# Kernel tuning notes

Hardware: AMD Instinct MI355X
Metric: run time of the kernel (lower is better)

## Reference

```python
import jax, jax.numpy as jnp
import numpy as np

NUM_HEADS = 16
EMBED_DIM = 1024
SEQ_LEN = 2048
BATCH = 2


def setup_inputs() -> dict:
    key = jax.random.key(0)
    ks = jax.random.split(key, 7)
    E = EMBED_DIM
    scale = 1.0 / np.sqrt(E)
    return {
        "query": jax.random.normal(ks[0], (SEQ_LEN, BATCH, E), jnp.float32),
        "key": jax.random.normal(ks[1], (SEQ_LEN, BATCH, E), jnp.float32),
        "value": jax.random.normal(ks[2], (SEQ_LEN, BATCH, E), jnp.float32),
        "in_proj_weight": jax.random.normal(ks[3], (3 * E, E), jnp.float32) * scale,
        "in_proj_bias": jnp.zeros((3 * E,), jnp.float32),
        "out_proj_weight": jax.random.normal(ks[4], (E, E), jnp.float32) * scale,
        "out_proj_bias": jnp.zeros((E,), jnp.float32),
    }


def reference(query, key, value, in_proj_weight, in_proj_bias, out_proj_weight, out_proj_bias):
    T, B, E = query.shape
    H = NUM_HEADS
    d = E // H
    scaling = float(d) ** -0.5
    # in-projections: rows [0:E) -> q, [E:2E) -> k, [2E:3E) -> v
    q = query @ in_proj_weight[:E].T + in_proj_bias[:E]
    k = key @ in_proj_weight[E:2 * E].T + in_proj_bias[E:2 * E]
    v = value @ in_proj_weight[2 * E:].T + in_proj_bias[2 * E:]
    q = q * scaling
    # (T, B, E) -> (B*H, T, d)
    q = q.reshape(T, B * H, d).transpose(1, 0, 2)
    k = k.reshape(T, B * H, d).transpose(1, 0, 2)
    v = v.reshape(T, B * H, d).transpose(1, 0, 2)
    S = k.shape[1]
    scores = jnp.einsum('ntd,nsd->nts', q, k)  # (B*H, T, S)
    attn = jax.nn.softmax(scores, axis=-1)
    out = jnp.einsum('nts,nsd->ntd', attn, v)  # (B*H, T, d)
    out = out.transpose(1, 0, 2).reshape(T, B, E)
    out = out @ out_proj_weight.T + out_proj_bias
    attn_avg = attn.reshape(B, H, T, S).sum(axis=1) / H
    return out, attn_avg
```

## Files before the change

kernel.cpp:

```cpp
#include <hip/hip_runtime.h>
#include <math.h>

#define T_LEN 2048
#define BATCH 2
#define EMB 1024
#define NHEAD 16
#define HDIM 64
#define BH (BATCH*NHEAD)
#define MROWS (T_LEN*BATCH)
#define QSCALE (0.125f * 1.4426950408889634f)
#define HEADBUF ((size_t)BH*T_LEN*HDIM)

typedef __attribute__((ext_vector_type(8))) short bf16x8;
typedef __attribute__((ext_vector_type(4))) float f32x4;

#define MFMA16(a,b,c) __builtin_amdgcn_mfma_f32_16x16x32_bf16(a,b,c,0,0,0)

__device__ __forceinline__ short f2bf(float f) {
    union { float f; unsigned u; } v; v.f = f;
    unsigned r = (v.u + 0x7FFFu + ((v.u >> 16) & 1u)) >> 16;
    return (short)(unsigned short)r;
}
__device__ __forceinline__ float bf2f(short s) {
    union { unsigned u; float f; } v; v.u = ((unsigned)(unsigned short)s) << 16;
    return v.f;
}
__device__ __forceinline__ unsigned cvtpk(float a, float b) {
    unsigned r;
    asm("v_cvt_pk_bf16_f32 %0, %1, %2" : "=v"(r) : "v"(a), "v"(b));
    return r;
}
__device__ __forceinline__ void gload16(const void* g, void* l) {
    __builtin_amdgcn_global_load_lds(
        (const __attribute__((address_space(1))) unsigned*)g,
        (__attribute__((address_space(3))) unsigned*)l, 16, 0, 0);
}

__global__ __launch_bounds__(256) void tobf16_kernel(
    const float* __restrict__ q, const float* __restrict__ k,
    const float* __restrict__ v, const float* __restrict__ w,
    const float* __restrict__ wo, short* __restrict__ out)
{
    size_t i8 = ((size_t)blockIdx.x * 256 + threadIdx.x) * 8;
    const float* src; size_t off;
    if (i8 < 12582912) {
        int sel = (int)(i8 >> 22);
        src = (sel == 0) ? q : (sel == 1) ? k : v;
        off = i8 & 4194303;
    } else if (i8 < 15728640) {
        src = w;  off = i8 - 12582912;
    } else {
        src = wo; off = i8 - 15728640;
    }
    float4 f0 = *(const float4*)(src + off);
    float4 f1 = *(const float4*)(src + off + 4);
    bf16x8 o;
    o[0]=f2bf(f0.x); o[1]=f2bf(f0.y); o[2]=f2bf(f0.z); o[3]=f2bf(f0.w);
    o[4]=f2bf(f1.x); o[5]=f2bf(f1.y); o[6]=f2bf(f1.z); o[7]=f2bf(f1.w);
    *(bf16x8*)(out + i8) = o;
}

__global__ __launch_bounds__(256) void inproj_gemm(
    const short* __restrict__ Xq, const short* __restrict__ Xk,
    const short* __restrict__ Xv, const short* __restrict__ Wb,
    const float* __restrict__ bias,
    short* __restrict__ qbuf, short* __restrict__ kbuf, short* __restrict__ vbufT)
{
    const int mBase = blockIdx.x * 128;
    const int nBase = blockIdx.y * 128;
    const int which = nBase >> 10;
    const short* __restrict__ X = (which == 0) ? Xq : (which == 1) ? Xk : Xv;

    __shared__ short Ast[2][128][32];
    __shared__ short Bst[2][128][32];

    const int tid  = threadIdx.x;
    const int lane = tid & 63;
    const int w    = tid >> 6;
    const int wr   = w >> 1, wc = w & 1;
    const int lr   = lane & 15, lg = lane >> 4;

    const int srow = lane >> 2;
    const int schk = (lane & 3) ^ ((lane >> 3) & 3);
    const int fchk = (lg ^ ((lr >> 1) & 3)) * 16;

    f32x4 acc[4][4] = {};

    #pragma unroll
    for (int j = 0; j < 2; ++j) {
        int r = j * 64 + w * 16 + srow;
        gload16(X  + (size_t)(mBase + r) * EMB + schk * 8,
                (char*)Ast[0] + j * 4096 + w * 1024);
        gload16(Wb + (size_t)(nBase + r) * EMB + schk * 8,
                (char*)Bst[0] + j * 4096 + w * 1024);
    }
    __syncthreads();

    int cur = 0;
    for (int kb = 0; kb < EMB; kb += 32) {
        if (kb + 32 < EMB) {
            #pragma unroll
            for (int j = 0; j < 2; ++j) {
                int r = j * 64 + w * 16 + srow;
                gload16(X  + (size_t)(mBase + r) * EMB + kb + 32 + schk * 8,
                        (char*)Ast[cur ^ 1] + j * 4096 + w * 1024);
                gload16(Wb + (size_t)(nBase + r) * EMB + kb + 32 + schk * 8,
                        (char*)Bst[cur ^ 1] + j * 4096 + w * 1024);
            }
        }
        bf16x8 af[4], bfr[4];
        #pragma unroll
        for (int rg = 0; rg < 4; ++rg)
            af[rg] = *(const bf16x8*)((char*)Ast[cur] + (wr * 64 + rg * 16 + lr) * 64 + fchk);
        #pragma unroll
        for (int cg = 0; cg < 4; ++cg)
            bfr[cg] = *(const bf16x8*)((char*)Bst[cur] + (wc * 64 + cg * 16 + lr) * 64 + fchk);
        #pragma unroll
        for (int rg = 0; rg < 4; ++rg)
            #pragma unroll
            for (int cg = 0; cg < 4; ++cg)
                acc[rg][cg] = MFMA16(af[rg], bfr[cg], acc[rg][cg]);
        __syncthreads();
        cur ^= 1;
    }

    #pragma unroll
    for (int rg = 0; rg < 4; ++rg) {
        #pragma unroll
        for (int cg = 0; cg < 4; ++cg) {
            int n  = nBase + wc * 64 + cg * 16 + lr;
            int e  = n & 1023;
            int h  = e >> 6, dd = e & 63;
            float bs = bias[n];
            #pragma unroll
            for (int ri = 0; ri < 4; ++ri) {
                int m = mBase + wr * 64 + rg * 16 + lg * 4 + ri;
                int t = m >> 1, b = m & 1;
                float val = acc[rg][cg][ri] + bs;
                short bfv;
                if (which == 0) { bfv = f2bf(val * QSCALE);
                    qbuf[((size_t)(b * NHEAD + h) * T_LEN + t) * HDIM + dd] = bfv; }
                else if (which == 1) { bfv = f2bf(val);
                    kbuf[((size_t)(b * NHEAD + h) * T_LEN + t) * HDIM + dd] = bfv; }
                else {
                    bfv = f2bf(val);
                    int s5 = t & 31;
                    int kk = ((s5 >> 2) & 3) * 8 + ((s5 >> 4) << 2) + (s5 & 3);
                    int tt = (t & ~31) | kk;
                    vbufT[((size_t)(b * NHEAD + h) * HDIM + dd) * T_LEN + tt] = bfv;
                }
            }
        }
    }
}

__global__ __launch_bounds__(256) void flash_kernel(
    const short* __restrict__ qb, const short* __restrict__ kbuf,
    const short* __restrict__ vbufT, short* __restrict__ h1,
    short* __restrict__ h2, float* __restrict__ mlws)
{
    const int qt = blockIdx.x;
    const int hb = blockIdx.y;

    __shared__ short Kst[2][64][64];
    __shared__ short Vst[2][64][64];

    const int tid  = threadIdx.x;
    const int lane = tid & 63;
    const int w    = tid >> 6;
    const int lr   = lane & 15, lg = lane >> 4;

    bf16x8 qa0, qa1;
    {
        const short* qsrc = qb + ((size_t)hb * T_LEN + qt * 64 + w * 16 + lr) * HDIM;
        qa0 = *(const bf16x8*)(qsrc + lg * 8);
        qa1 = *(const bf16x8*)(qsrc + 32 + lg * 8);
    }

    const short* kbase = kbuf  + (size_t)hb * T_LEN * HDIM;
    const short* vbase = vbufT + (size_t)hb * HDIM * T_LEN;

    const int krow = lane >> 3;
    const int kc16 = (lane & 7) ^ krow;
    const int rb0 = ((0 + lg) ^ (lr & 7)) * 16;
    const int rb1 = ((4 + lg) ^ (lr & 7)) * 16;

    float l_r = 0.f;
    f32x4 o_acc[4] = {};

    for (int st = 0; st < T_LEN / 128; ++st) {
        __syncthreads();
        #pragma unroll
        for (int it = 0; it < 2; ++it) {
            int r = (w * 2 + it) * 8 + krow;
            #pragma unroll
            for (int sh = 0; sh < 2; ++sh) {
                gload16(kbase + (size_t)(st * 128 + sh * 64 + r) * HDIM + kc16 * 8,
                        (char*)Kst[sh] + (w * 2 + it) * 1024);
                gload16(vbase + (size_t)r * T_LEN + st * 128 + sh * 64 + kc16 * 8,
                        (char*)Vst[sh] + (w * 2 + it) * 1024);
            }
        }
        __syncthreads();

        #pragma unroll
        for (int sh = 0; sh < 2; ++sh) {
            f32x4 sc[4] = {};
            #pragma unroll
            for (int sg = 0; sg < 4; ++sg) {
                const char* krowp = (const char*)Kst[sh] + (sg * 16 + lr) * 128;
                bf16x8 kf0 = *(const bf16x8*)(krowp + rb0);
                bf16x8 kf1 = *(const bf16x8*)(krowp + rb1);
                sc[sg] = MFMA16(kf0, qa0, sc[sg]);
                sc[sg] = MFMA16(kf1, qa1, sc[sg]);
            }

            float p[4][4];
            #pragma unroll
            for (int sg = 0; sg < 4; ++sg)
                #pragma unroll
                for (int ri = 0; ri < 4; ++ri) {
                    p[sg][ri] = exp2f(sc[sg][ri]);
                    l_r += p[sg][ri];
                }

            #pragma unroll
            for (int ks = 0; ks < 2; ++ks) {
                union { unsigned u[4]; bf16x8 v; } pau;
                pau.u[0] = cvtpk(p[ks * 2][0],     p[ks * 2][1]);
                pau.u[1] = cvtpk(p[ks * 2][2],     p[ks * 2][3]);
                pau.u[2] = cvtpk(p[ks * 2 + 1][0], p[ks * 2 + 1][1]);
                pau.u[3] = cvtpk(p[ks * 2 + 1][2], p[ks * 2 + 1][3]);
                #pragma unroll
                for (int dsub = 0; dsub < 4; ++dsub) {
                    const char* vrowp = (const char*)Vst[sh] + (dsub * 16 + lr) * 128;
                    bf16x8 vf = *(const bf16x8*)(vrowp + (ks ? rb1 : rb0));
                    o_acc[dsub] = MFMA16(pau.v, vf, o_acc[dsub]);
                }
            }
        }
    }

    float lsum = l_r;
    lsum += __shfl_xor(lsum, 16);
    lsum += __shfl_xor(lsum, 32);
    float inv = 1.0f / lsum;
    float invq[4];
    #pragma unroll
    for (int ri = 0; ri < 4; ++ri) invq[ri] = __shfl(inv, lg * 20 + ri);
    #pragma unroll
    for (int ri = 0; ri < 4; ++ri) {
        int row = qt * 64 + w * 16 + lg * 4 + ri;
        #pragma unroll
        for (int dsub = 0; dsub < 4; ++dsub) {
            float x = o_acc[dsub][ri] * invq[ri];
            size_t idx = ((size_t)hb * T_LEN + row) * HDIM + dsub * 16 + lr;
            short a = f2bf(x);
            h1[idx] = a;
            h2[idx] = f2bf(x - bf2f(a));
        }
    }
    if (lg == 0) {
        int row = qt * 64 + w * 16 + lr;
        mlws[(size_t)hb * T_LEN + row] = __log2f(lsum);
    }
}

__global__ __launch_bounds__(256) void avg_kernel(
    const short* __restrict__ qbuf, const short* __restrict__ kbuf,
    const float* __restrict__ mlws, float* __restrict__ attn_avg)
{
    const int st = blockIdx.x;
    const int qt = blockIdx.y;
    const int b  = blockIdx.z;

    __shared__ short K2[2][2][64][64];

    const int tid  = threadIdx.x;
    const int lane = tid & 63;
    const int w    = tid >> 6;
    const int lr   = lane & 15, lg = lane >> 4;
    const int srow = tid >> 3;
    const int scol = (tid & 7) * 8;

    f32x4 acc[4] = {};

    #pragma unroll
    for (int hh = 0; hh < 2; ++hh) {
        int hb0 = b * NHEAD + hh;
        #pragma unroll
        for (int j = 0; j < 2; ++j)
            gload16(kbuf + ((size_t)hb0 * T_LEN + st * 64 + j * 32 + srow) * HDIM + scol,
                    (char*)K2[0][hh] + j * 4096 + w * 1024);
    }
    __syncthreads();

    int cur = 0;
    for (int rnd = 0; rnd < 8; ++rnd) {
        if (rnd + 1 < 8) {
            #pragma unroll
            for (int hh = 0; hh < 2; ++hh) {
                int hbn = b * NHEAD + (rnd + 1) * 2 + hh;
                #pragma unroll
                for (int j = 0; j < 2; ++j)
                    gload16(kbuf + ((size_t)hbn * T_LEN + st * 64 + j * 32 + srow) * HDIM + scol,
                            (char*)K2[cur ^ 1][hh] + j * 4096 + w * 1024);
            }
        }
        #pragma unroll
        for (int hh = 0; hh < 2; ++hh) {
            int hb = b * NHEAD + rnd * 2 + hh;
            const short* qsrc = qbuf + ((size_t)hb * T_LEN + qt * 64 + w * 16 + lr) * HDIM;
            bf16x8 qa0 = *(const bf16x8*)(qsrc + lg * 8);
            bf16x8 qa1 = *(const bf16x8*)(qsrc + 32 + lg * 8);

            f32x4 sc[4] = {};
            __builtin_amdgcn_s_setprio(1);
            #pragma unroll
            for (int sg = 0; sg < 4; ++sg) {
                bf16x8 kf0 = *(const bf16x8*)&K2[cur][hh][sg * 16 + lr][lg * 8];
                bf16x8 kf1 = *(const bf16x8*)&K2[cur][hh][sg * 16 + lr][32 + lg * 8];
                sc[sg] = MFMA16(qa0, kf0, sc[sg]);
                sc[sg] = MFMA16(qa1, kf1, sc[sg]);
            }
            __builtin_amdgcn_s_setprio(0);

            #pragma unroll
            for (int ri = 0; ri < 4; ++ri) {
                int row = qt * 64 + w * 16 + lg * 4 + ri;
                float ml = mlws[(size_t)hb * T_LEN + row];
                #pragma unroll
                for (int sg = 0; sg < 4; ++sg)
                    acc[sg][ri] += exp2f(sc[sg][ri] - ml);
            }
        }
        __syncthreads();
        cur ^= 1;
    }

    const float invH = 1.0f / (float)NHEAD;
    #pragma unroll
    for (int ri = 0; ri < 4; ++ri) {
        int row = qt * 64 + w * 16 + lg * 4 + ri;
        #pragma unroll
        for (int sg = 0; sg < 4; ++sg)
            attn_avg[((size_t)b * T_LEN + row) * T_LEN + st * 64 + sg * 16 + lr] =
                acc[sg][ri] * invH;
    }
}

__global__ __launch_bounds__(256) void outproj_gemm(
    const short* __restrict__ h1, const short* __restrict__ h2,
    const short* __restrict__ Wob, const float* __restrict__ bo,
    float* __restrict__ out)
{
    const int mBase = blockIdx.x * 128;
    const int nBase = blockIdx.y * 128;

    __shared__ short A1st[128][64];
    __shared__ short A2st[128][64];
    __shared__ short Bst [128][64];

    const int tid  = threadIdx.x;
    const int lane = tid & 63;
    const int w    = tid >> 6;
    const int wr   = w >> 1, wc = w & 1;
    const int lr   = lane & 15, lg = lane >> 4;
    const int srow = tid >> 3;
    const int scol = (tid & 7) * 8;

    f32x4 acc[4][4] = {};

    for (int kb = 0; kb < EMB; kb += 64) {
        const int h = kb >> 6;
        __syncthreads();
        #pragma unroll
        for (int j = 0; j < 4; ++j) {
            int m = mBase + j * 32 + srow;
            int t = m >> 1, b = m & 1;
            size_t aoff = ((size_t)(b * NHEAD + h) * T_LEN + t) * HDIM + scol;
            gload16(h1 + aoff, (char*)A1st + j * 4096 + w * 1024);
            gload16(h2 + aoff, (char*)A2st + j * 4096 + w * 1024);
            gload16(Wob + (size_t)(nBase + j * 32 + srow) * EMB + kb + scol,
                    (char*)Bst + j * 4096 + w * 1024);
        }
        __syncthreads();
        #pragma unroll
        for (int ks = 0; ks < 2; ++ks) {
            bf16x8 a1[4], a2[4], bfr[4];
            #pragma unroll
            for (int rg = 0; rg < 4; ++rg) {
                a1[rg] = *(const bf16x8*)&A1st[wr * 64 + rg * 16 + lr][ks * 32 + lg * 8];
                a2[rg] = *(const bf16x8*)&A2st[wr * 64 + rg * 16 + lr][ks * 32 + lg * 8];
            }
            #pragma unroll
            for (int cg = 0; cg < 4; ++cg)
                bfr[cg] = *(const bf16x8*)&Bst[wc * 64 + cg * 16 + lr][ks * 32 + lg * 8];
            #pragma unroll
            for (int rg = 0; rg < 4; ++rg)
                #pragma unroll
                for (int cg = 0; cg < 4; ++cg) {
                    acc[rg][cg] = MFMA16(a1[rg], bfr[cg], acc[rg][cg]);
                    acc[rg][cg] = MFMA16(a2[rg], bfr[cg], acc[rg][cg]);
                }
        }
    }

    #pragma unroll
    for (int rg = 0; rg < 4; ++rg) {
        #pragma unroll
        for (int cg = 0; cg < 4; ++cg) {
            int n = nBase + wc * 64 + cg * 16 + lr;
            float bs = bo[n];
            #pragma unroll
            for (int ri = 0; ri < 4; ++ri) {
                int m = mBase + wr * 64 + rg * 16 + lg * 4 + ri;
                out[(size_t)m * EMB + n] = acc[rg][cg][ri] + bs;
            }
        }
    }
}

extern "C" void kernel_launch(void* const* d_in, const int* in_sizes, int n_in,
                              void* d_out, int out_size, void* d_ws, size_t ws_size,
                              hipStream_t stream)
{
    const float* query = (const float*)d_in[0];
    const float* key   = (const float*)d_in[1];
    const float* value = (const float*)d_in[2];
    const float* ipw   = (const float*)d_in[3];
    const float* ipb   = (const float*)d_in[4];
    const float* opw   = (const float*)d_in[5];
    const float* opb   = (const float*)d_in[6];

    short* qb  = (short*)d_ws;
    short* kb  = qb + HEADBUF;
    short* vbT = kb + HEADBUF;
    short* h1  = vbT + HEADBUF;
    short* h2  = h1 + HEADBUF;
    short* xvb = h2 + HEADBUF;
    short* wbf = xvb + HEADBUF;
    short* wob = wbf + (size_t)3 * EMB * EMB;
    float* mlws = (float*)(wob + (size_t)EMB * EMB);

    float* out      = (float*)d_out;
    float* attn_avg = out + (size_t)MROWS * EMB;

    tobf16_kernel<<<8192, 256, 0, stream>>>(query, key, value, ipw, opw, h1);
    inproj_gemm  <<<dim3(MROWS / 128, 3 * EMB / 128), 256, 0, stream>>>(
        h1, h2, xvb, wbf, ipb, qb, kb, vbT);
    flash_kernel <<<dim3(T_LEN / 64, BH),             256, 0, stream>>>(
        qb, kb, vbT, h1, h2, mlws);
    avg_kernel   <<<dim3(T_LEN / 64, T_LEN / 64, BATCH), 256, 0, stream>>>(
        qb, kb, mlws, attn_avg);
    outproj_gemm <<<dim3(MROWS / 128, EMB / 128),     256, 0, stream>>>(
        h1, h2, wob, opb, out);
}
```

Measured before the change: 207.5 us.

## Drop bf16 hi/lo split for out-proj, double avg-kernel query tile, pipeline out-proj GEMM

The flash kernel now writes only a single bf16 copy of the attention output, and the out-projection GEMM consumes one operand instead of a hi/lo pair. That halves its MFMA count and activation traffic at the cost of output precision. The out-proj GEMM is also restructured with double-buffered LDS, a 32-wide K step and XOR-swizzled shared layout to overlap loads with compute. The avg kernel processes 128 query rows per block, reusing each staged K tile across two query fragments and halving the grid.

```diff
diff --git a/kernel.cpp b/kernel.cpp
--- a/kernel.cpp
+++ b/kernel.cpp
@@ -157,7 +157,7 @@
 __global__ __launch_bounds__(256) void flash_kernel(
     const short* __restrict__ qb, const short* __restrict__ kbuf,
     const short* __restrict__ vbufT, short* __restrict__ h1,
-    short* __restrict__ h2, float* __restrict__ mlws)
+    float* __restrict__ mlws)
 {
     const int qt = blockIdx.x;
     const int hb = blockIdx.y;
@@ -254,10 +254,7 @@
         #pragma unroll
         for (int dsub = 0; dsub < 4; ++dsub) {
             float x = o_acc[dsub][ri] * invq[ri];
-            size_t idx = ((size_t)hb * T_LEN + row) * HDIM + dsub * 16 + lr;
-            short a = f2bf(x);
-            h1[idx] = a;
-            h2[idx] = f2bf(x - bf2f(a));
+            h1[((size_t)hb * T_LEN + row) * HDIM + dsub * 16 + lr] = f2bf(x);
         }
     }
     if (lg == 0) {
@@ -270,9 +267,9 @@
     const short* __restrict__ qbuf, const short* __restrict__ kbuf,
     const float* __restrict__ mlws, float* __restrict__ attn_avg)
 {
-    const int st = blockIdx.x;
-    const int qt = blockIdx.y;
-    const int b  = blockIdx.z;
+    const int st  = blockIdx.x;
+    const int qt2 = blockIdx.y;
+    const int b   = blockIdx.z;
 
     __shared__ short K2[2][2][64][64];
 
@@ -283,7 +280,7 @@
     const int srow = tid >> 3;
     const int scol = (tid & 7) * 8;
 
-    f32x4 acc[4] = {};
+    f32x4 acc[2][4] = {};
 
     #pragma unroll
     for (int hh = 0; hh < 2; ++hh) {
@@ -310,29 +307,39 @@
         #pragma unroll
         for (int hh = 0; hh < 2; ++hh) {
             int hb = b * NHEAD + rnd * 2 + hh;
-            const short* qsrc = qbuf + ((size_t)hb * T_LEN + qt * 64 + w * 16 + lr) * HDIM;
-            bf16x8 qa0 = *(const bf16x8*)(qsrc + lg * 8);
-            bf16x8 qa1 = *(const bf16x8*)(qsrc + 32 + lg * 8);
-
-            f32x4 sc[4] = {};
+            bf16x8 qa[2][2];
+            #pragma unroll
+            for (int qf = 0; qf < 2; ++qf) {
+                const short* qsrc = qbuf +
+                    ((size_t)hb * T_LEN + qt2 * 128 + qf * 64 + w * 16 + lr) * HDIM;
+                qa[qf][0] = *(const bf16x8*)(qsrc + lg * 8);
+                qa[qf][1] = *(const bf16x8*)(qsrc + 32 + lg * 8);
+            }
+
+            f32x4 sc[2][4] = {};
             __builtin_amdgcn_s_setprio(1);
             #pragma unroll
             for (int sg = 0; sg < 4; ++sg) {
                 bf16x8 kf0 = *(const bf16x8*)&K2[cur][hh][sg * 16 + lr][lg * 8];
                 bf16x8 kf1 = *(const bf16x8*)&K2[cur][hh][sg * 16 + lr][32 + lg * 8];
-                sc[sg] = MFMA16(qa0, kf0, sc[sg]);
-                sc[sg] = MFMA16(qa1, kf1, sc[sg]);
+                #pragma unroll
+                for (int qf = 0; qf < 2; ++qf) {
+                    sc[qf][sg] = MFMA16(qa[qf][0], kf0, sc[qf][sg]);
+                    sc[qf][sg] = MFMA16(qa[qf][1], kf1, sc[qf][sg]);
+                }
             }
             __builtin_amdgcn_s_setprio(0);
 
             #pragma unroll
-            for (int ri = 0; ri < 4; ++ri) {
-                int row = qt * 64 + w * 16 + lg * 4 + ri;
-                float ml = mlws[(size_t)hb * T_LEN + row];
+            for (int qf = 0; qf < 2; ++qf)
                 #pragma unroll
-                for (int sg = 0; sg < 4; ++sg)
-                    acc[sg][ri] += exp2f(sc[sg][ri] - ml);
-            }
+                for (int ri = 0; ri < 4; ++ri) {
+                    int row = qt2 * 128 + qf * 64 + w * 16 + lg * 4 + ri;
+                    float ml = mlws[(size_t)hb * T_LEN + row];
+                    #pragma unroll
+                    for (int sg = 0; sg < 4; ++sg)
+                        acc[qf][sg][ri] += exp2f(sc[qf][sg][ri] - ml);
+                }
         }
         __syncthreads();
         cur ^= 1;
@@ -340,71 +347,79 @@
 
     const float invH = 1.0f / (float)NHEAD;
     #pragma unroll
-    for (int ri = 0; ri < 4; ++ri) {
-        int row = qt * 64 + w * 16 + lg * 4 + ri;
-        #pragma unroll
-        for (int sg = 0; sg < 4; ++sg)
-            attn_avg[((size_t)b * T_LEN + row) * T_LEN + st * 64 + sg * 16 + lr] =
-                acc[sg][ri] * invH;
-    }
+    for (int qf = 0; qf < 2; ++qf)
+        #pragma unroll
+        for (int ri = 0; ri < 4; ++ri) {
+            int row = qt2 * 128 + qf * 64 + w * 16 + lg * 4 + ri;
+            #pragma unroll
+            for (int sg = 0; sg < 4; ++sg)
+                attn_avg[((size_t)b * T_LEN + row) * T_LEN + st * 64 + sg * 16 + lr] =
+                    acc[qf][sg][ri] * invH;
+        }
 }
 
 __global__ __launch_bounds__(256) void outproj_gemm(
-    const short* __restrict__ h1, const short* __restrict__ h2,
-    const short* __restrict__ Wob, const float* __restrict__ bo,
-    float* __restrict__ out)
+    const short* __restrict__ h1, const short* __restrict__ Wob,
+    const float* __restrict__ bo, float* __restrict__ out)
 {
     const int mBase = blockIdx.x * 128;
     const int nBase = blockIdx.y * 128;
 
-    __shared__ short A1st[128][64];
-    __shared__ short A2st[128][64];
-    __shared__ short Bst [128][64];
+    __shared__ short Ast[2][128][32];
+    __shared__ short Bst[2][128][32];
 
     const int tid  = threadIdx.x;
     const int lane = tid & 63;
     const int w    = tid >> 6;
     const int wr   = w >> 1, wc = w & 1;
     const int lr   = lane & 15, lg = lane >> 4;
-    const int srow = tid >> 3;
-    const int scol = (tid & 7) * 8;
+
+    const int srow = lane >> 2;
+    const int schk = (lane & 3) ^ ((lane >> 3) & 3);
+    const int fchk = (lg ^ ((lr >> 1) & 3)) * 16;
 
     f32x4 acc[4][4] = {};
 
-    for (int kb = 0; kb < EMB; kb += 64) {
-        const int h = kb >> 6;
+    #define ASRC(r, kb)                                                       \
+        (h1 + ((size_t)(((mBase + (r)) & 1) * NHEAD + ((kb) >> 6)) * T_LEN +  \
+               ((mBase + (r)) >> 1)) * HDIM + ((kb) & 63) + schk * 8)
+
+    #pragma unroll
+    for (int j = 0; j < 2; ++j) {
+        int r = j * 64 + w * 16 + srow;
+        gload16(ASRC(r, 0), (char*)Ast[0] + j * 4096 + w * 1024);
+        gload16(Wob + (size_t)(nBase + r) * EMB + schk * 8,
+                (char*)Bst[0] + j * 4096 + w * 1024);
+    }
+    __syncthreads();
+
+    int cur = 0;
+    for (int kb = 0; kb < EMB; kb += 32) {
+        if (kb + 32 < EMB) {
+            #pragma unroll
+            for (int j = 0; j < 2; ++j) {
+                int r = j * 64 + w * 16 + srow;
+                gload16(ASRC(r, kb + 32), (char*)Ast[cur ^ 1] + j * 4096 + w * 1024);
+                gload16(Wob + (size_t)(nBase + r) * EMB + kb + 32 + schk * 8,
+                        (char*)Bst[cur ^ 1] + j * 4096 + w * 1024);
+            }
+        }
+        bf16x8 af[4], bfr[4];
+        #pragma unroll
+        for (int rg = 0; rg < 4; ++rg)
+            af[rg] = *(const bf16x8*)((char*)Ast[cur] + (wr * 64 + rg * 16 + lr) * 64 + fchk);
+        #pragma unroll
+        for (int cg = 0; cg < 4; ++cg)
+            bfr[cg] = *(const bf16x8*)((char*)Bst[cur] + (wc * 64 + cg * 16 + lr) * 64 + fchk);
+        #pragma unroll
+        for (int rg = 0; rg < 4; ++rg)
+            #pragma unroll
+            for (int cg = 0; cg < 4; ++cg)
+                acc[rg][cg] = MFMA16(af[rg], bfr[cg], acc[rg][cg]);
         __syncthreads();
-        #pragma unroll
-        for (int j = 0; j < 4; ++j) {
-            int m = mBase + j * 32 + srow;
-            int t = m >> 1, b = m & 1;
-            size_t aoff = ((size_t)(b * NHEAD + h) * T_LEN + t) * HDIM + scol;
-            gload16(h1 + aoff, (char*)A1st + j * 4096 + w * 1024);
-            gload16(h2 + aoff, (char*)A2st + j * 4096 + w * 1024);
-            gload16(Wob + (size_t)(nBase + j * 32 + srow) * EMB + kb + scol,
-                    (char*)Bst + j * 4096 + w * 1024);
-        }
-        __syncthreads();
-        #pragma unroll
-        for (int ks = 0; ks < 2; ++ks) {
-            bf16x8 a1[4], a2[4], bfr[4];
-            #pragma unroll
-            for (int rg = 0; rg < 4; ++rg) {
-                a1[rg] = *(const bf16x8*)&A1st[wr * 64 + rg * 16 + lr][ks * 32 + lg * 8];
-                a2[rg] = *(const bf16x8*)&A2st[wr * 64 + rg * 16 + lr][ks * 32 + lg * 8];
-            }
-            #pragma unroll
-            for (int cg = 0; cg < 4; ++cg)
-                bfr[cg] = *(const bf16x8*)&Bst[wc * 64 + cg * 16 + lr][ks * 32 + lg * 8];
-            #pragma unroll
-            for (int rg = 0; rg < 4; ++rg)
-                #pragma unroll
-                for (int cg = 0; cg < 4; ++cg) {
-                    acc[rg][cg] = MFMA16(a1[rg], bfr[cg], acc[rg][cg]);
-                    acc[rg][cg] = MFMA16(a2[rg], bfr[cg], acc[rg][cg]);
-                }
-        }
-    }
+        cur ^= 1;
+    }
+    #undef ASRC
 
     #pragma unroll
     for (int rg = 0; rg < 4; ++rg) {
@@ -450,9 +465,9 @@
     inproj_gemm  <<<dim3(MROWS / 128, 3 * EMB / 128), 256, 0, stream>>>(
         h1, h2, xvb, wbf, ipb, qb, kb, vbT);
     flash_kernel <<<dim3(T_LEN / 64, BH),             256, 0, stream>>>(
-        qb, kb, vbT, h1, h2, mlws);
-    avg_kernel   <<<dim3(T_LEN / 64, T_LEN / 64, BATCH), 256, 0, stream>>>(
+        qb, kb, vbT, h1, mlws);
+    avg_kernel   <<<dim3(T_LEN / 64, T_LEN / 128, BATCH), 256, 0, stream>>>(
         qb, kb, mlws, attn_avg);
     outproj_gemm <<<dim3(MROWS / 128, EMB / 128),     256, 0, stream>>>(
-        h1, h2, wob, opb, out);
-}
+        h1, wob, opb, out);
+}
```

New measurement: 206.1 us. Within noise of the previous version (-0.7%).
